# Kernel optimization log

Hardware: AMD Instinct MI355X
Metric: run time of the kernel (lower is better)

## Reference

```python
import jax, jax.numpy as jnp
import numpy as np

B, S, NH, DM, REPR, FF = 256, 110, 12, 768, 1024, 3072
HD = DM // NH  # 64
LN_EPS = 1e-12


def setup_inputs() -> dict:
    key = jax.random.key(0)
    ks = jax.random.split(key, 20)
    s = 0.02
    inp = {
        'im_repr': jax.random.normal(ks[0], (B, REPR), jnp.float32),
        'q_repr':  jax.random.normal(ks[1], (B, S, DM), jnp.float32),
        # self-attention projections (768 -> 768)
        'Wq1': jax.random.normal(ks[2], (DM, DM), jnp.float32) * s,
        'bq1': jnp.zeros((DM,), jnp.float32),
        'Wk1': jax.random.normal(ks[3], (DM, DM), jnp.float32) * s,
        'bk1': jnp.zeros((DM,), jnp.float32),
        'Wv1': jax.random.normal(ks[4], (DM, DM), jnp.float32) * s,
        'bv1': jnp.zeros((DM,), jnp.float32),
        # cross-attention: query from 768, key/value from encoder width 1024
        'Wq2': jax.random.normal(ks[5], (DM, DM), jnp.float32) * s,
        'bq2': jnp.zeros((DM,), jnp.float32),
        'Wk2': jax.random.normal(ks[6], (REPR, DM), jnp.float32) * s,
        'bk2': jnp.zeros((DM,), jnp.float32),
        'Wv2': jax.random.normal(ks[7], (REPR, DM), jnp.float32) * s,
        'bv2': jnp.zeros((DM,), jnp.float32),
        # FFN (768 -> 3072 -> 768) + LayerNorm
        'W1': jax.random.normal(ks[8], (DM, FF), jnp.float32) * s,
        'b1': jnp.zeros((FF,), jnp.float32),
        'W2': jax.random.normal(ks[9], (FF, DM), jnp.float32) * s,
        'b2': jnp.zeros((DM,), jnp.float32),
        'ln_g': jnp.ones((DM,), jnp.float32),
        'ln_b': jnp.zeros((DM,), jnp.float32),
    }
    return inp


def _heads(x):
    # [B, L, DM] -> [B, NH, L, HD]
    b, l, _ = x.shape
    return x.reshape(b, l, NH, HD).transpose(0, 2, 1, 3)


def _attn(hq, hkv, Wq, bq, Wk, bk, Wv, bv):
    # scaled dot-product attention (the source's relative-position bias is dead
    # code: attention_scores is overwritten by a fresh QK^T before scaling)
    q = _heads(hq @ Wq + bq)      # [B,NH,Lq,HD]
    k = _heads(hkv @ Wk + bk)     # [B,NH,Lk,HD]
    v = _heads(hkv @ Wv + bv)
    scores = jnp.einsum('bhqd,bhkd->bhqk', q, k) / np.sqrt(HD).astype(np.float32)
    probs = jax.nn.softmax(scores, axis=-1)
    ctx = jnp.einsum('bhqk,bhkd->bhqd', probs, v)
    b, _, lq, _ = ctx.shape
    return ctx.transpose(0, 2, 1, 3).reshape(b, lq, DM)


def reference(im_repr, q_repr, Wq1, bq1, Wk1, bk1, Wv1, bv1,
              Wq2, bq2, Wk2, bk2, Wv2, bv2, W1, b1, W2, b2, ln_g, ln_b):
    # self-attention over query tokens
    q_attn = _attn(q_repr, q_repr, Wq1, bq1, Wk1, bk1, Wv1, bv1)
    # image representation broadcast across the S key/value positions
    vision = jnp.broadcast_to(im_repr[:, None, :], (B, S, REPR))
    x = _attn(q_attn, vision, Wq2, bq2, Wk2, bk2, Wv2, bv2).mean(axis=1)  # [B,DM]
    # FFN + residual + LayerNorm (dropout = identity in eval)
    h = jax.nn.gelu(x @ W1 + b1, approximate=False) @ W2 + b2
    y = x + h
    mu = y.mean(axis=-1, keepdims=True)
    var = ((y - mu) ** 2).mean(axis=-1, keepdims=True)
    return (y - mu) / jnp.sqrt(var + LN_EPS) * ln_g + ln_b
```

## Files before the change

### kernel.cpp

```cpp
#include <hip/hip_runtime.h>
#include <hip/hip_bf16.h>
#include <math.h>

#define BATCH 256
#define DM    768
#define REPR  1024
#define FF    3072

typedef __attribute__((ext_vector_type(8))) short bf16x8;
typedef __attribute__((ext_vector_type(4))) float f32x4;

__device__ __forceinline__ unsigned bf16rne(float f){
  union{float f; unsigned u;} x; x.f = f;
  return (x.u + 0x7FFFu + ((x.u >> 16) & 1u)) >> 16;
}
__device__ __forceinline__ unsigned pk2(float lo, float hi){
  return bf16rne(lo) | (bf16rne(hi) << 16);
}

__global__ __launch_bounds__(256)
void gemm_g1(const float* __restrict__ Wv2, const float* __restrict__ im,
             float* __restrict__ P1)
{
  const int z = blockIdx.z, bx = blockIdx.x, by = blockIdx.y;
  const int tid = threadIdx.x;
  const int lane = tid & 63, wid = tid >> 6;
  const int wr = wid >> 1, wc = wid & 1;
  const int arow = by * 32 + wr * 16 + (lane & 15);
  const int colb = bx * 64 + wc * 32;
  const int kq8  = (lane >> 4) * 8;
  const int kb   = z * 256;

  const float* apf  = im + (size_t)arow * REPR + kb + kq8;
  const int c0 = colb + (lane & 15), c1 = c0 + 16;
  const float* wrow = Wv2 + (size_t)(kb + kq8) * DM;

  f32x4 acc0 = (f32x4)(0.0f), acc1 = (f32x4)(0.0f);
  float4 a0c = *(const float4*)apf, a1c = *(const float4*)(apf + 4);
  float b0c[8], b1c[8];
  #pragma unroll
  for (int j = 0; j < 8; ++j) {
    b0c[j] = wrow[(size_t)j * DM + c0];
    b1c[j] = wrow[(size_t)j * DM + c1];
  }

  for (int s = 0; s < 8; ++s) {
    float4 a0n, a1n; float b0n[8], b1n[8];
    const bool more = (s + 1) < 8;
    if (more) {
      const float* a2 = apf + (s + 1) * 32;
      a0n = *(const float4*)a2; a1n = *(const float4*)(a2 + 4);
      const float* w2r = wrow + (size_t)(s + 1) * 32 * DM;
      #pragma unroll
      for (int j = 0; j < 8; ++j) {
        b0n[j] = w2r[(size_t)j * DM + c0];
        b1n[j] = w2r[(size_t)j * DM + c1];
      }
    }
    union U { unsigned u[4]; bf16x8 v; } afr, bfr0, bfr1;
    afr.u[0] = pk2(a0c.x, a0c.y); afr.u[1] = pk2(a0c.z, a0c.w);
    afr.u[2] = pk2(a1c.x, a1c.y); afr.u[3] = pk2(a1c.z, a1c.w);
    #pragma unroll
    for (int j = 0; j < 4; ++j) {
      bfr0.u[j] = pk2(b0c[2*j], b0c[2*j+1]);
      bfr1.u[j] = pk2(b1c[2*j], b1c[2*j+1]);
    }
    acc0 = __builtin_amdgcn_mfma_f32_16x16x32_bf16(afr.v, bfr0.v, acc0, 0, 0, 0);
    acc1 = __builtin_amdgcn_mfma_f32_16x16x32_bf16(afr.v, bfr1.v, acc1, 0, 0, 0);
    if (more) {
      a0c = a0n; a1c = a1n;
      #pragma unroll
      for (int j = 0; j < 8; ++j) { b0c[j] = b0n[j]; b1c[j] = b1n[j]; }
    }
  }

  const int crow = by * 32 + wr * 16 + (lane >> 4) * 4;
  float* dst = P1 + (size_t)z * BATCH * DM;
  #pragma unroll
  for (int nf = 0; nf < 2; ++nf) {
    const int c = colb + nf * 16 + (lane & 15);
    const f32x4 a = nf ? acc1 : acc0;
    #pragma unroll
    for (int r = 0; r < 4; ++r)
      dst[(size_t)(crow + r) * DM + c] = a[r];
  }
}

__global__ __launch_bounds__(256)
void fixup_x(const float* __restrict__ P1, const float* __restrict__ bv2,
             float* __restrict__ xf, ushort* __restrict__ xbf)
{
  const int e = (blockIdx.x * 256 + threadIdx.x) * 4;
  const int c = e % DM;
  float4 s = *(const float4*)(P1 + e);
  #pragma unroll
  for (int z = 1; z < 4; ++z) {
    float4 v = *(const float4*)(P1 + (size_t)z * BATCH * DM + e);
    s.x += v.x; s.y += v.y; s.z += v.z; s.w += v.w;
  }
  float4 bb = *(const float4*)(bv2 + c);
  s.x += bb.x; s.y += bb.y; s.z += bb.z; s.w += bb.w;
  *(float4*)(xf + e) = s;
  uint2 o = { pk2(s.x, s.y), pk2(s.z, s.w) };
  *(uint2*)(xbf + e) = o;
}

__global__ __launch_bounds__(256)
void gemm_g2(const ushort* __restrict__ xbf, const float* __restrict__ W1,
             const float* __restrict__ b1, ushort* __restrict__ tbf)
{
  int id = blockIdx.y * 48 + blockIdx.x;
  id = (id & 7) * 48 + (id >> 3);
  const int bx = id / 8, by = id % 8;

  const int lane = threadIdx.x & 63, wid = threadIdx.x >> 6;
  const int wr = wid >> 1, wc = wid & 1;
  const int arow = by * 32 + wr * 16 + (lane & 15);
  const int colb = bx * 64 + wc * 32;
  const int kq = (lane >> 4) * 8;

  const ushort* ap = xbf + (size_t)arow * DM + kq;
  const int c0 = colb + (lane & 15), c1 = c0 + 16;
  const float* wrow = W1 + (size_t)kq * FF;

  f32x4 acc0 = (f32x4)(0.0f), acc1 = (f32x4)(0.0f);
  union U { uint4 q; bf16x8 v; };
  U a_c;
  a_c.q = *(const uint4*)ap;
  float b0c[8], b1c[8];
  #pragma unroll
  for (int j = 0; j < 8; ++j) {
    b0c[j] = wrow[(size_t)j * FF + c0];
    b1c[j] = wrow[(size_t)j * FF + c1];
  }

  for (int t = 0; t < 24; ++t) {
    U a_n; float b0n[8], b1n[8];
    const bool more = (t + 1) < 24;
    if (more) {
      a_n.q = *(const uint4*)(ap + (t + 1) * 32);
      const float* w2r = wrow + (size_t)(t + 1) * 32 * FF;
      #pragma unroll
      for (int j = 0; j < 8; ++j) {
        b0n[j] = w2r[(size_t)j * FF + c0];
        b1n[j] = w2r[(size_t)j * FF + c1];
      }
    }
    union V { unsigned u[4]; bf16x8 v; } bfr0, bfr1;
    #pragma unroll
    for (int j = 0; j < 4; ++j) {
      bfr0.u[j] = pk2(b0c[2*j], b0c[2*j+1]);
      bfr1.u[j] = pk2(b1c[2*j], b1c[2*j+1]);
    }
    acc0 = __builtin_amdgcn_mfma_f32_16x16x32_bf16(a_c.v, bfr0.v, acc0, 0, 0, 0);
    acc1 = __builtin_amdgcn_mfma_f32_16x16x32_bf16(a_c.v, bfr1.v, acc1, 0, 0, 0);
    if (more) {
      a_c = a_n;
      #pragma unroll
      for (int j = 0; j < 8; ++j) { b0c[j] = b0n[j]; b1c[j] = b1n[j]; }
    }
  }

  const int crow = by * 32 + wr * 16 + (lane >> 4) * 4;
  #pragma unroll
  for (int nf = 0; nf < 2; ++nf) {
    const int c = colb + nf * 16 + (lane & 15);
    const f32x4 a = nf ? acc1 : acc0;
    #pragma unroll
    for (int r = 0; r < 4; ++r) {
      float v = a[r] + b1[c];
      v = 0.5f * v * (1.0f + erff(v * 0.70710678118654752f));
      tbf[(size_t)(crow + r) * FF + c] = (ushort)bf16rne(v);
    }
  }
}

__global__ __launch_bounds__(256)
void gemm_g3(const ushort* __restrict__ tbf, const float* __restrict__ W2,
             float* __restrict__ P3)
{
  int id = blockIdx.y * 12 + blockIdx.x;
  id = (id & 7) * 12 + (id >> 3);
  const int bx = id / 8, by = id % 8;

  const int lane = threadIdx.x & 63, wid = threadIdx.x >> 6;
  const int wr = wid >> 1, wc = wid & 1;
  const int arow = by * 32 + wr * 16 + (lane & 15);
  const int colb = bx * 64 + wc * 32;
  const int kq = (lane >> 4) * 8;
  const int kb = blockIdx.z * 384;

  const ushort* ap = tbf + (size_t)arow * FF + kb + kq;
  const int c0 = colb + (lane & 15), c1 = c0 + 16;
  const float* wrow = W2 + (size_t)(kb + kq) * DM;

  f32x4 acc0 = (f32x4)(0.0f), acc1 = (f32x4)(0.0f);
  union U { uint4 q; bf16x8 v; };
  U a_c;
  a_c.q = *(const uint4*)ap;
  float b0c[8], b1c[8];
  #pragma unroll
  for (int j = 0; j < 8; ++j) {
    b0c[j] = wrow[(size_t)j * DM + c0];
    b1c[j] = wrow[(size_t)j * DM + c1];
  }

  for (int t = 0; t < 12; ++t) {
    U a_n; float b0n[8], b1n[8];
    const bool more = (t + 1) < 12;
    if (more) {
      a_n.q = *(const uint4*)(ap + (t + 1) * 32);
      const float* w2r = wrow + (size_t)(t + 1) * 32 * DM;
      #pragma unroll
      for (int j = 0; j < 8; ++j) {
        b0n[j] = w2r[(size_t)j * DM + c0];
        b1n[j] = w2r[(size_t)j * DM + c1];
      }
    }
    union V { unsigned u[4]; bf16x8 v; } bfr0, bfr1;
    #pragma unroll
    for (int j = 0; j < 4; ++j) {
      bfr0.u[j] = pk2(b0c[2*j], b0c[2*j+1]);
      bfr1.u[j] = pk2(b1c[2*j], b1c[2*j+1]);
    }
    acc0 = __builtin_amdgcn_mfma_f32_16x16x32_bf16(a_c.v, bfr0.v, acc0, 0, 0, 0);
    acc1 = __builtin_amdgcn_mfma_f32_16x16x32_bf16(a_c.v, bfr1.v, acc1, 0, 0, 0);
    if (more) {
      a_c = a_n;
      #pragma unroll
      for (int j = 0; j < 8; ++j) { b0c[j] = b0n[j]; b1c[j] = b1n[j]; }
    }
  }

  const int crow = by * 32 + wr * 16 + (lane >> 4) * 4;
  float* dst = P3 + (size_t)blockIdx.z * BATCH * DM;
  #pragma unroll
  for (int nf = 0; nf < 2; ++nf) {
    const int c = colb + nf * 16 + (lane & 15);
    const f32x4 a = nf ? acc1 : acc0;
    #pragma unroll
    for (int r = 0; r < 4; ++r)
      dst[(size_t)(crow + r) * DM + c] = a[r];
  }
}

__global__ __launch_bounds__(256)
void ln_final(const float* __restrict__ P3, const float* __restrict__ xf,
              const float* __restrict__ b2, const float* __restrict__ g,
              const float* __restrict__ be, float* __restrict__ out)
{
  const int row = blockIdx.x, tid = threadIdx.x;
  const int lane = tid & 63, wave = tid >> 6;

  float v[3];
  #pragma unroll
  for (int i = 0; i < 3; ++i) {
    const int c = tid + i * 256;
    float s = xf[(size_t)row * DM + c] + b2[c];
    #pragma unroll
    for (int z = 0; z < 8; ++z) s += P3[((size_t)z * BATCH + row) * DM + c];
    v[i] = s;
  }

  __shared__ float red[4];
  float s = v[0] + v[1] + v[2];
  #pragma unroll
  for (int o = 32; o > 0; o >>= 1) s += __shfl_down(s, o);
  if (lane == 0) red[wave] = s;
  __syncthreads();
  const float mu = (red[0] + red[1] + red[2] + red[3]) * (1.0f / 768.0f);
  __syncthreads();
  const float d0 = v[0] - mu, d1 = v[1] - mu, d2 = v[2] - mu;
  float q = d0*d0 + d1*d1 + d2*d2;
  #pragma unroll
  for (int o = 32; o > 0; o >>= 1) q += __shfl_down(q, o);
  if (lane == 0) red[wave] = q;
  __syncthreads();
  const float var = (red[0] + red[1] + red[2] + red[3]) * (1.0f / 768.0f);
  const float inv = rsqrtf(var + 1e-12f);

  float* o = out + (size_t)row * DM;
  o[tid      ] = d0 * inv * g[tid      ] + be[tid      ];
  o[tid + 256] = d1 * inv * g[tid + 256] + be[tid + 256];
  o[tid + 512] = d2 * inv * g[tid + 512] + be[tid + 512];
}

extern "C" void kernel_launch(void* const* d_in, const int* in_sizes, int n_in,
                              void* d_out, int out_size, void* d_ws, size_t ws_size,
                              hipStream_t stream)
{
  const float* im  = (const float*)d_in[0];
  const float* Wv2 = (const float*)d_in[12];
  const float* bv2 = (const float*)d_in[13];
  const float* W1  = (const float*)d_in[14];
  const float* b1  = (const float*)d_in[15];
  const float* W2  = (const float*)d_in[16];
  const float* b2  = (const float*)d_in[17];
  const float* g   = (const float*)d_in[18];
  const float* be  = (const float*)d_in[19];
  float* out = (float*)d_out;

  char* w = (char*)d_ws;
  ushort* xbf = (ushort*)(w);
  ushort* tbf = (ushort*)(w + 393216);
  float*  xf  = (float*) (w + 1966080);
  float*  P1  = (float*) (w + 2752512);
  float*  P3  = (float*) (w + 5898240);

  gemm_g1<<<dim3(12, 8, 4), 256, 0, stream>>>(Wv2, im, P1);
  fixup_x<<<192, 256, 0, stream>>>(P1, bv2, xf, xbf);
  gemm_g2<<<dim3(48, 8, 1), 256, 0, stream>>>(xbf, W1, b1, tbf);
  gemm_g3<<<dim3(12, 8, 8), 256, 0, stream>>>(tbf, W2, P3);
  ln_final<<<BATCH, 256, 0, stream>>>(P3, xf, b2, g, be, out);
}
```

Before: 44.88 us.

## Fuse split-K reduction and bf16 conversion into FFN1 GEMM prologue

Removes the separate fixup kernel: each gemm_g2f block sums the four split-K partials of P1 plus bias for its 32 rows, converts to bf16, and stores them in swizzled shared memory used as the A operand. ln_final recomputes the residual x from P1 instead of reading a stored copy. This saves a kernel launch and the intermediate buffers, but each of the 48 column blocks redundantly re-reduces the same rows and uses 48KB of LDS, which may limit occupancy.

```diff
diff --git a/kernel.cpp b/kernel.cpp
--- a/kernel.cpp
+++ b/kernel.cpp
@@ -87,46 +87,55 @@
 }
 
 __global__ __launch_bounds__(256)
-void fixup_x(const float* __restrict__ P1, const float* __restrict__ bv2,
-             float* __restrict__ xf, ushort* __restrict__ xbf)
-{
-  const int e = (blockIdx.x * 256 + threadIdx.x) * 4;
-  const int c = e % DM;
-  float4 s = *(const float4*)(P1 + e);
-  #pragma unroll
-  for (int z = 1; z < 4; ++z) {
-    float4 v = *(const float4*)(P1 + (size_t)z * BATCH * DM + e);
-    s.x += v.x; s.y += v.y; s.z += v.z; s.w += v.w;
-  }
-  float4 bb = *(const float4*)(bv2 + c);
-  s.x += bb.x; s.y += bb.y; s.z += bb.z; s.w += bb.w;
-  *(float4*)(xf + e) = s;
-  uint2 o = { pk2(s.x, s.y), pk2(s.z, s.w) };
-  *(uint2*)(xbf + e) = o;
-}
-
-__global__ __launch_bounds__(256)
-void gemm_g2(const ushort* __restrict__ xbf, const float* __restrict__ W1,
-             const float* __restrict__ b1, ushort* __restrict__ tbf)
-{
+void gemm_g2f(const float* __restrict__ P1, const float* __restrict__ bv2,
+              const float* __restrict__ W1, const float* __restrict__ b1,
+              ushort* __restrict__ tbf)
+{
+  __shared__ uint4 xs[3072];
+
   int id = blockIdx.y * 48 + blockIdx.x;
   id = (id & 7) * 48 + (id >> 3);
   const int bx = id / 8, by = id % 8;
-
-  const int lane = threadIdx.x & 63, wid = threadIdx.x >> 6;
+  const int tid = threadIdx.x;
+
+  const size_t SL = (size_t)BATCH * DM;
+  #pragma unroll
+  for (int i = 0; i < 12; ++i) {
+    const int gidx = tid + i * 256;
+    const int r = gidx / 96, o = gidx % 96;
+    const size_t e = (size_t)(by * 32 + r) * DM + o * 8;
+    float4 s0 = *(const float4*)(P1 + e);
+    float4 s1 = *(const float4*)(P1 + e + 4);
+    #pragma unroll
+    for (int z = 1; z < 4; ++z) {
+      float4 v0 = *(const float4*)(P1 + (size_t)z * SL + e);
+      float4 v1 = *(const float4*)(P1 + (size_t)z * SL + e + 4);
+      s0.x += v0.x; s0.y += v0.y; s0.z += v0.z; s0.w += v0.w;
+      s1.x += v1.x; s1.y += v1.y; s1.z += v1.z; s1.w += v1.w;
+    }
+    float4 bb0 = *(const float4*)(bv2 + o * 8);
+    float4 bb1 = *(const float4*)(bv2 + o * 8 + 4);
+    s0.x += bb0.x; s0.y += bb0.y; s0.z += bb0.z; s0.w += bb0.w;
+    s1.x += bb1.x; s1.y += bb1.y; s1.z += bb1.z; s1.w += bb1.w;
+    uint4 wv = { pk2(s0.x, s0.y), pk2(s0.z, s0.w),
+                 pk2(s1.x, s1.y), pk2(s1.z, s1.w) };
+    xs[r * 96 + (o ^ (r & 7))] = wv;
+  }
+  __syncthreads();
+
+  const int lane = tid & 63, wid = tid >> 6;
   const int wr = wid >> 1, wc = wid & 1;
-  const int arow = by * 32 + wr * 16 + (lane & 15);
+  const int rloc = wr * 16 + (lane & 15);
   const int colb = bx * 64 + wc * 32;
+  const int c0 = colb + (lane & 15), c1 = c0 + 16;
   const int kq = (lane >> 4) * 8;
-
-  const ushort* ap = xbf + (size_t)arow * DM + kq;
-  const int c0 = colb + (lane & 15), c1 = c0 + 16;
+  const int xbase = rloc * 96, xm = rloc & 7, xq = lane >> 4;
   const float* wrow = W1 + (size_t)kq * FF;
 
   f32x4 acc0 = (f32x4)(0.0f), acc1 = (f32x4)(0.0f);
   union U { uint4 q; bf16x8 v; };
   U a_c;
-  a_c.q = *(const uint4*)ap;
+  a_c.q = xs[xbase + (xq ^ xm)];
   float b0c[8], b1c[8];
   #pragma unroll
   for (int j = 0; j < 8; ++j) {
@@ -138,7 +147,7 @@
     U a_n; float b0n[8], b1n[8];
     const bool more = (t + 1) < 24;
     if (more) {
-      a_n.q = *(const uint4*)(ap + (t + 1) * 32);
+      a_n.q = xs[xbase + ((xq + 4 * (t + 1)) ^ xm)];
       const float* w2r = wrow + (size_t)(t + 1) * 32 * FF;
       #pragma unroll
       for (int j = 0; j < 8; ++j) {
@@ -245,9 +254,10 @@
 }
 
 __global__ __launch_bounds__(256)
-void ln_final(const float* __restrict__ P3, const float* __restrict__ xf,
-              const float* __restrict__ b2, const float* __restrict__ g,
-              const float* __restrict__ be, float* __restrict__ out)
+void ln_final(const float* __restrict__ P1, const float* __restrict__ bv2,
+              const float* __restrict__ P3, const float* __restrict__ b2,
+              const float* __restrict__ g, const float* __restrict__ be,
+              float* __restrict__ out)
 {
   const int row = blockIdx.x, tid = threadIdx.x;
   const int lane = tid & 63, wave = tid >> 6;
@@ -256,7 +266,11 @@
   #pragma unroll
   for (int i = 0; i < 3; ++i) {
     const int c = tid + i * 256;
-    float s = xf[(size_t)row * DM + c] + b2[c];
+    float x = P1[(size_t)row * DM + c];
+    #pragma unroll
+    for (int z = 1; z < 4; ++z) x += P1[((size_t)z * BATCH + row) * DM + c];
+    x += bv2[c];
+    float s = x + b2[c];
     #pragma unroll
     for (int z = 0; z < 8; ++z) s += P3[((size_t)z * BATCH + row) * DM + c];
     v[i] = s;
@@ -301,15 +315,12 @@
   float* out = (float*)d_out;
 
   char* w = (char*)d_ws;
-  ushort* xbf = (ushort*)(w);
-  ushort* tbf = (ushort*)(w + 393216);
-  float*  xf  = (float*) (w + 1966080);
-  float*  P1  = (float*) (w + 2752512);
-  float*  P3  = (float*) (w + 5898240);
+  float*  P1  = (float*) (w);
+  ushort* tbf = (ushort*)(w + 3145728);
+  float*  P3  = (float*) (w + 4718592);
 
   gemm_g1<<<dim3(12, 8, 4), 256, 0, stream>>>(Wv2, im, P1);
-  fixup_x<<<192, 256, 0, stream>>>(P1, bv2, xf, xbf);
-  gemm_g2<<<dim3(48, 8, 1), 256, 0, stream>>>(xbf, W1, b1, tbf);
+  gemm_g2f<<<dim3(48, 8, 1), 256, 0, stream>>>(P1, bv2, W1, b1, tbf);
   gemm_g3<<<dim3(12, 8, 8), 256, 0, stream>>>(tbf, W2, P3);
-  ln_final<<<BATCH, 256, 0, stream>>>(P3, xf, b2, g, be, out);
-}
+  ln_final<<<BATCH, 256, 0, stream>>>(P1, bv2, P3, b2, g, be, out);
+}
```

New measurement: 53.33 us. 18.8% more time.
